# Kernel tuning notes

Hardware: AMD Instinct MI355X
Metric: run time of the kernel (lower is better)

The kernel has to match this reference:

```python
import jax, jax.numpy as jnp
import numpy as np

N = 50000      # nodes
E = 1600000    # edges (avg degree 32)
IN = 128       # input feature dim
H = 4          # heads
C = 16         # out channels per head
NEG_SLOPE = 0.2


def setup_inputs() -> dict:
    key = jax.random.key(0)
    k = jax.random.split(key, 6)
    x = jax.random.normal(k[0], (N, IN), jnp.float32)
    edge_index = jax.random.randint(k[1], (2, E), 0, N, dtype=jnp.int32).astype(jnp.int64)
    W = jax.random.normal(k[2], (H * C, IN), jnp.float32) * (1.0 / np.sqrt(IN))
    att_src = jax.random.normal(k[3], (H, C), jnp.float32) * 0.1
    att_dst = jax.random.normal(k[4], (H, C), jnp.float32) * 0.1
    bias = jax.random.normal(k[5], (H * C,), jnp.float32) * 0.01
    return {"x": x, "edge_index": edge_index, "W": W,
            "att_src": att_src, "att_dst": att_dst, "bias": bias}


def reference(x, edge_index, W, att_src, att_dst, bias):
    # shared linear projection (PyG GATConv lin, no bias): [N, H, C]
    xp = (x @ W.T).reshape(-1, H, C)
    # per-node attention logits: [N, H]
    a_src = jnp.einsum('nhc,hc->nh', xp, att_src)
    a_dst = jnp.einsum('nhc,hc->nh', xp, att_dst)
    src, dst = edge_index[0], edge_index[1]  # messages flow src(j) -> dst(i)
    # per-edge scores: [E, H]
    e = jax.nn.leaky_relu(a_src[src] + a_dst[dst], negative_slope=NEG_SLOPE)
    # segment softmax over destination neighborhoods
    m = jax.ops.segment_max(e, dst, num_segments=N)           # [N, H]
    m = jnp.where(jnp.isfinite(m), m, 0.0)                     # empty segments
    ex = jnp.exp(e - m[dst])
    s = jax.ops.segment_sum(ex, dst, num_segments=N)           # [N, H]
    alpha = ex / (s[dst] + 1e-16)                              # [E, H]
    # weighted messages, scatter-add to destinations
    msg = (alpha[:, :, None] * xp[src]).reshape(E, H * C)      # [E, H*C]
    out = jax.ops.segment_sum(msg, dst, num_segments=N)        # [N, H*C]
    return out + bias
```

## Files before the change

### kernel.cpp

```cpp
#include <hip/hip_runtime.h>
#include <hip/hip_bf16.h>
#include <math.h>

#define N_NODES 50000
#define N_EDGES 1600000
#define IN_DIM  128
#define HC      64
#define NH      4
#define SLOTS   72
#define BSHIFT  6
#define BNODES  64
#define NB      782
#define BCAP    2432
#define BIN_BLOCKS 64
#define BIN_G   6250
#define BIN_IT  13
#define GEMM_BLOCKS 391
#define GEMM_LDS 33792

__global__ __launch_bounds__(512) void bin_kernel(
    const int* __restrict__ ei, int* __restrict__ gcursor,
    unsigned int* __restrict__ barr) {
    __shared__ int lcount[NB], lbase[NB], lcnt2[NB];
    int tid = (int)threadIdx.x;
    int bx  = (int)blockIdx.x;
    for (int j = tid; j < NB; j += 512) { lcount[j] = 0; lcnt2[j] = 0; }
    __syncthreads();
    const int4* sp = (const int4*)ei;
    const int4* dp = (const int4*)(ei + N_EDGES);
    int g0 = bx * BIN_G;

    for (int it = 0; it < BIN_IT; ++it) {
        int gi = it * 512 + tid;
        if (gi < BIN_G) {
            int4 dv = dp[g0 + gi];
            atomicAdd(&lcount[dv.x >> BSHIFT], 1);
            atomicAdd(&lcount[dv.y >> BSHIFT], 1);
            atomicAdd(&lcount[dv.z >> BSHIFT], 1);
            atomicAdd(&lcount[dv.w >> BSHIFT], 1);
        }
    }
    __syncthreads();
    for (int j = tid; j < NB; j += 512) {
        int c = lcount[j];
        lbase[j] = (c > 0) ? atomicAdd(&gcursor[j], c) : 0;
    }
    __syncthreads();
    for (int it = 0; it < BIN_IT; ++it) {
        int gi = it * 512 + tid;
        if (gi < BIN_G) {
            int4 sv = sp[g0 + gi];
            int4 dv = dp[g0 + gi];
            int s[4] = {sv.x, sv.y, sv.z, sv.w};
            int d[4] = {dv.x, dv.y, dv.z, dv.w};
#pragma unroll
            for (int u = 0; u < 4; ++u) {
                int bk = d[u] >> BSHIFT;
                int lp = atomicAdd(&lcnt2[bk], 1);
                int pos = lbase[bk] + lp;
                if (pos < BCAP)
                    barr[(size_t)bk * BCAP + pos] =
                        (unsigned)s[u] | ((unsigned)(d[u] & (BNODES - 1)) << 20);
            }
        }
    }
}

__global__ __launch_bounds__(512) void gemm_kernel(
    const float* __restrict__ x, const float* __restrict__ W,
    const float* __restrict__ att_src, const float* __restrict__ att_dst,
    __hip_bfloat16* __restrict__ xp, float* __restrict__ a_src,
    float* __restrict__ a_dst) {
    extern __shared__ char smraw[];
    int tid = (int)threadIdx.x;
    int gb  = (int)blockIdx.x;
    float* Wl = (float*)smraw;
    const float4* W4 = (const float4*)W;
#pragma unroll
    for (int j = 0; j < 4; ++j) {
        int f = j * 512 + tid;
        int c = f >> 5, k4 = f & 31;
        *(float4*)&Wl[c * 132 + k4 * 4] = W4[f];
    }
    __syncthreads();

    int l = tid & 63, w = tid >> 6, q = l >> 4, i = l & 15;
    int n0 = gb * 128 + w * 16 + q * 4;
    int nj[4];
#pragma unroll
    for (int j = 0; j < 4; ++j) {
        int n = n0 + j;
        nj[j] = (n < N_NODES) ? n : N_NODES - 1;
    }
    const float* wlp = Wl + i * 132;
    float4 acc[4] = {{0,0,0,0},{0,0,0,0},{0,0,0,0},{0,0,0,0}};
    float4 xr[4], xn[4];
#pragma unroll
    for (int j = 0; j < 4; ++j) xr[j] = *(const float4*)(x + (size_t)nj[j] * IN_DIM);
#pragma unroll 2
    for (int k0 = 0; k0 < IN_DIM; k0 += 4) {
        if (k0 + 4 < IN_DIM) {
#pragma unroll
            for (int j = 0; j < 4; ++j)
                xn[j] = *(const float4*)(x + (size_t)nj[j] * IN_DIM + k0 + 4);
        }
        float4 wl0 = *(const float4*)(wlp + 0 * 16 * 132 + k0);
        float4 wl1 = *(const float4*)(wlp + 1 * 16 * 132 + k0);
        float4 wl2 = *(const float4*)(wlp + 2 * 16 * 132 + k0);
        float4 wl3 = *(const float4*)(wlp + 3 * 16 * 132 + k0);
#pragma unroll
        for (int j = 0; j < 4; ++j) {
            float4 xv = xr[j];
            acc[j].x = fmaf(xv.x, wl0.x, fmaf(xv.y, wl0.y, fmaf(xv.z, wl0.z, fmaf(xv.w, wl0.w, acc[j].x))));
            acc[j].y = fmaf(xv.x, wl1.x, fmaf(xv.y, wl1.y, fmaf(xv.z, wl1.z, fmaf(xv.w, wl1.w, acc[j].y))));
            acc[j].z = fmaf(xv.x, wl2.x, fmaf(xv.y, wl2.y, fmaf(xv.z, wl2.z, fmaf(xv.w, wl2.w, acc[j].z))));
            acc[j].w = fmaf(xv.x, wl3.x, fmaf(xv.y, wl3.y, fmaf(xv.z, wl3.z, fmaf(xv.w, wl3.w, acc[j].w))));
        }
#pragma unroll
        for (int j = 0; j < 4; ++j) xr[j] = xn[j];
    }

    float a_s0 = att_src[i], a_s1 = att_src[16 + i], a_s2 = att_src[32 + i], a_s3 = att_src[48 + i];
    float a_d0 = att_dst[i], a_d1 = att_dst[16 + i], a_d2 = att_dst[32 + i], a_d3 = att_dst[48 + i];
#pragma unroll
    for (int j = 0; j < 4; ++j) {
        int n = n0 + j;
        if (n < N_NODES) {
            __hip_bfloat16* xw = xp + (size_t)n * HC;
            xw[i]      = __float2bfloat16(acc[j].x);
            xw[16 + i] = __float2bfloat16(acc[j].y);
            xw[32 + i] = __float2bfloat16(acc[j].z);
            xw[48 + i] = __float2bfloat16(acc[j].w);
            float4 ps, pd;
            ps.x = acc[j].x * a_s0; ps.y = acc[j].y * a_s1;
            ps.z = acc[j].z * a_s2; ps.w = acc[j].w * a_s3;
            pd.x = acc[j].x * a_d0; pd.y = acc[j].y * a_d1;
            pd.z = acc[j].z * a_d2; pd.w = acc[j].w * a_d3;
#pragma unroll
            for (int off = 1; off < 16; off <<= 1) {
                ps.x += __shfl_xor(ps.x, off, 64); ps.y += __shfl_xor(ps.y, off, 64);
                ps.z += __shfl_xor(ps.z, off, 64); ps.w += __shfl_xor(ps.w, off, 64);
                pd.x += __shfl_xor(pd.x, off, 64); pd.y += __shfl_xor(pd.y, off, 64);
                pd.z += __shfl_xor(pd.z, off, 64); pd.w += __shfl_xor(pd.w, off, 64);
            }
            if (i == 0) {
                *(float4*)(a_src + n * NH) = ps;
                *(float4*)(a_dst + n * NH) = pd;
            }
        }
    }
}

__global__ __launch_bounds__(512) void fused_gather_kernel(
    const unsigned int* __restrict__ barr, const int* __restrict__ gcursor,
    const float* __restrict__ a_src, const float* __restrict__ a_dst,
    const __hip_bfloat16* __restrict__ xp, const float* __restrict__ bias,
    float* __restrict__ out) {
    __shared__ int lcsr[BNODES * SLOTS];
    __shared__ int deg[BNODES];
    int b = blockIdx.x, tid = (int)threadIdx.x;
    if (tid < BNODES) deg[tid] = 0;
    __syncthreads();
    int n = gcursor[b];
    n = (n < BCAP) ? n : BCAP;
    const unsigned int* src = barr + (size_t)b * BCAP;

    for (int i0 = 0; i0 < n; i0 += 2048) {
        int ibase = i0 + tid * 4;
        unsigned v[4]; bool val[4]; int dp[4], pos[4];
        if (ibase < n) {
            uint4 r = *(const uint4*)(src + ibase);
            v[0] = r.x; v[1] = r.y; v[2] = r.z; v[3] = r.w;
        } else { v[0] = v[1] = v[2] = v[3] = 0u; }
#pragma unroll
        for (int u = 0; u < 4; ++u) {
            val[u] = (ibase + u) < n;
            dp[u] = (int)(v[u] >> 20);
            if (val[u]) pos[u] = atomicAdd(&deg[dp[u]], 1);
        }
#pragma unroll
        for (int u = 0; u < 4; ++u)
            if (val[u] && pos[u] < SLOTS)
                lcsr[dp[u] * SLOTS + pos[u]] = (int)(v[u] & 0xFFFFF);
    }
    __syncthreads();

    int l = tid & 63;
    int w = tid >> 6;
    int g = l >> 3;
    int i = l & 7;
    int h = i >> 1;
    int dl = w * 8 + g;
    int dst = (b << BSHIFT) + dl;
    int dg = deg[dl];
    dg = (dg < SLOTS) ? dg : SLOTS;
    int dstc = (dst < N_NODES) ? dst : 0;
    float adh = a_dst[dstc * NH + h];

    int sreg[9];
#pragma unroll
    for (int k = 0; k < 9; ++k) sreg[k] = lcsr[dl * SLOTS + k * 8 + i];

    const unsigned short* xpi = (const unsigned short*)xp + 8 * i;
    const float* asrch = a_src + h;
    int gsel = l & 56;
    float a0=0,a1=0,a2=0,a3=0,a4=0,a5=0,a6=0,a7=0;
    float dsum = 0.f;

#pragma unroll
    for (int k = 0; k < 9; ++k) {
        if (dg > k * 8) {
            int cnt = dg - k * 8;
            int reg = sreg[k];
            int s8[8]; float g8[8]; uint4 t8[8];
#pragma unroll
            for (int u = 0; u < 8; ++u) {
                int raw = __shfl(reg, gsel | u, 64);
                s8[u] = (u < cnt) ? raw : 0;
            }
#pragma unroll
            for (int u = 0; u < 8; ++u) g8[u] = asrch[s8[u] * NH];
#pragma unroll
            for (int u = 0; u < 8; ++u)
                t8[u] = *(const uint4*)(xpi + (size_t)s8[u] * HC);
#pragma unroll
            for (int u = 0; u < 8; ++u) {
                float e = g8[u] + adh;
                e = fmaxf(e, 0.2f * e);
                float wv = (u < cnt) ? __expf(e) : 0.f;
                dsum += wv;
                uint4 t = t8[u];
                a0 = fmaf(wv, __uint_as_float(t.x << 16),          a0);
                a1 = fmaf(wv, __uint_as_float(t.x & 0xffff0000u),  a1);
                a2 = fmaf(wv, __uint_as_float(t.y << 16),          a2);
                a3 = fmaf(wv, __uint_as_float(t.y & 0xffff0000u),  a3);
                a4 = fmaf(wv, __uint_as_float(t.z << 16),          a4);
                a5 = fmaf(wv, __uint_as_float(t.z & 0xffff0000u),  a5);
                a6 = fmaf(wv, __uint_as_float(t.w << 16),          a6);
                a7 = fmaf(wv, __uint_as_float(t.w & 0xffff0000u),  a7);
            }
        }
    }
    if (dst < N_NODES) {
        float inv = 1.f / (dsum + 1e-16f);
        float4 b0 = *(const float4*)(bias + 8 * i);
        float4 b1 = *(const float4*)(bias + 8 * i + 4);
        float4 o0, o1;
        o0.x = a0 * inv + b0.x; o0.y = a1 * inv + b0.y;
        o0.z = a2 * inv + b0.z; o0.w = a3 * inv + b0.w;
        o1.x = a4 * inv + b1.x; o1.y = a5 * inv + b1.y;
        o1.z = a6 * inv + b1.z; o1.w = a7 * inv + b1.w;
        float* op = out + (size_t)dst * HC + 8 * i;
        *(float4*)op = o0;
        *(float4*)(op + 4) = o1;
    }
}

extern "C" void kernel_launch(void* const* d_in, const int* in_sizes, int n_in,
                              void* d_out, int out_size, void* d_ws, size_t ws_size,
                              hipStream_t stream) {
    const float* x       = (const float*)d_in[0];
    const int*   ei      = (const int*)d_in[1];
    const float* W       = (const float*)d_in[2];
    const float* att_src = (const float*)d_in[3];
    const float* att_dst = (const float*)d_in[4];
    const float* bias    = (const float*)d_in[5];
    float* out = (float*)d_out;

    char* ws = (char*)d_ws;
    __hip_bfloat16* xp      = (__hip_bfloat16*)(ws);
    float*          a_srcv  = (float*)(ws + 6400000);
    float*          a_dstv  = (float*)(ws + 7200000);
    int*            gcursor = (int*)  (ws + 8000000);
    unsigned int*   barr    = (unsigned int*)(ws + 8016384);

    hipMemsetAsync(gcursor, 0, NB * sizeof(int), stream);
    bin_kernel<<<BIN_BLOCKS, 512, 0, stream>>>(ei, gcursor, barr);
    gemm_kernel<<<GEMM_BLOCKS, 512, GEMM_LDS, stream>>>(
        x, W, att_src, att_dst, xp, a_srcv, a_dstv);
    fused_gather_kernel<<<NB, 512, 0, stream>>>(barr, gcursor,
                                                a_srcv, a_dstv, xp, bias, out);
}
```

Before: 167.8 us.

## Split edge binning into count, scan and append kernels with more blocks

Replaces the single binning kernel, which used 64 blocks and global atomic cursors, with three kernels. A per-block count pass, a per-bucket exclusive scan across blocks, and an append pass that writes at precomputed offsets. Block count rises from 64 to 250 to fill more of the GPU, and the memset and global atomics go away. The cost is two extra kernel launches, a second read of the destination indices, and a counts/base matrix in workspace. Bucket order within a bin also becomes deterministic.

```diff
diff --git a/kernel.cpp b/kernel.cpp
--- a/kernel.cpp
+++ b/kernel.cpp
@@ -12,25 +12,22 @@
 #define BNODES  64
 #define NB      782
 #define BCAP    2432
-#define BIN_BLOCKS 64
-#define BIN_G   6250
-#define BIN_IT  13
+#define BIN_BLOCKS 250
+#define BIN_G   1600
 #define GEMM_BLOCKS 391
 #define GEMM_LDS 33792
 
-__global__ __launch_bounds__(512) void bin_kernel(
-    const int* __restrict__ ei, int* __restrict__ gcursor,
-    unsigned int* __restrict__ barr) {
-    __shared__ int lcount[NB], lbase[NB], lcnt2[NB];
+__global__ __launch_bounds__(512) void bin_count_kernel(
+    const int* __restrict__ ei, int* __restrict__ counts) {
+    __shared__ int lcount[NB];
     int tid = (int)threadIdx.x;
     int bx  = (int)blockIdx.x;
-    for (int j = tid; j < NB; j += 512) { lcount[j] = 0; lcnt2[j] = 0; }
-    __syncthreads();
-    const int4* sp = (const int4*)ei;
+    for (int j = tid; j < NB; j += 512) lcount[j] = 0;
+    __syncthreads();
     const int4* dp = (const int4*)(ei + N_EDGES);
     int g0 = bx * BIN_G;
-
-    for (int it = 0; it < BIN_IT; ++it) {
+#pragma unroll
+    for (int it = 0; it < 4; ++it) {
         int gi = it * 512 + tid;
         if (gi < BIN_G) {
             int4 dv = dp[g0 + gi];
@@ -41,12 +38,45 @@
         }
     }
     __syncthreads();
+    for (int j = tid; j < NB; j += 512)
+        counts[bx * NB + j] = lcount[j];
+}
+
+__global__ __launch_bounds__(256) void bin_scan_kernel(
+    const int* __restrict__ counts, int* __restrict__ base,
+    int* __restrict__ btot) {
+    __shared__ int sc[256];
+    int j = (int)blockIdx.x, t = (int)threadIdx.x;
+    int v = (t < BIN_BLOCKS) ? counts[t * NB + j] : 0;
+    sc[t] = v;
+    __syncthreads();
+#pragma unroll
+    for (int off = 1; off < 256; off <<= 1) {
+        int u = (t >= off) ? sc[t - off] : 0;
+        __syncthreads();
+        sc[t] += u;
+        __syncthreads();
+    }
+    if (t < BIN_BLOCKS) base[t * NB + j] = sc[t] - v;
+    if (t == BIN_BLOCKS - 1) btot[j] = sc[t];
+}
+
+__global__ __launch_bounds__(512) void bin_append_kernel(
+    const int* __restrict__ ei, const int* __restrict__ base,
+    unsigned int* __restrict__ barr) {
+    __shared__ int lbase[NB], lcnt[NB];
+    int tid = (int)threadIdx.x;
+    int bx  = (int)blockIdx.x;
     for (int j = tid; j < NB; j += 512) {
-        int c = lcount[j];
-        lbase[j] = (c > 0) ? atomicAdd(&gcursor[j], c) : 0;
-    }
-    __syncthreads();
-    for (int it = 0; it < BIN_IT; ++it) {
+        lbase[j] = base[bx * NB + j];
+        lcnt[j]  = 0;
+    }
+    __syncthreads();
+    const int4* sp = (const int4*)ei;
+    const int4* dp = (const int4*)(ei + N_EDGES);
+    int g0 = bx * BIN_G;
+#pragma unroll
+    for (int it = 0; it < 4; ++it) {
         int gi = it * 512 + tid;
         if (gi < BIN_G) {
             int4 sv = sp[g0 + gi];
@@ -56,7 +86,7 @@
 #pragma unroll
             for (int u = 0; u < 4; ++u) {
                 int bk = d[u] >> BSHIFT;
-                int lp = atomicAdd(&lcnt2[bk], 1);
+                int lp = atomicAdd(&lcnt[bk], 1);
                 int pos = lbase[bk] + lp;
                 if (pos < BCAP)
                     barr[(size_t)bk * BCAP + pos] =
@@ -152,7 +182,7 @@
 }
 
 __global__ __launch_bounds__(512) void fused_gather_kernel(
-    const unsigned int* __restrict__ barr, const int* __restrict__ gcursor,
+    const unsigned int* __restrict__ barr, const int* __restrict__ btot,
     const float* __restrict__ a_src, const float* __restrict__ a_dst,
     const __hip_bfloat16* __restrict__ xp, const float* __restrict__ bias,
     float* __restrict__ out) {
@@ -161,7 +191,7 @@
     int b = blockIdx.x, tid = (int)threadIdx.x;
     if (tid < BNODES) deg[tid] = 0;
     __syncthreads();
-    int n = gcursor[b];
+    int n = btot[b];
     n = (n < BCAP) ? n : BCAP;
     const unsigned int* src = barr + (size_t)b * BCAP;
 
@@ -271,13 +301,16 @@
     __hip_bfloat16* xp      = (__hip_bfloat16*)(ws);
     float*          a_srcv  = (float*)(ws + 6400000);
     float*          a_dstv  = (float*)(ws + 7200000);
-    int*            gcursor = (int*)  (ws + 8000000);
+    int*            btot    = (int*)  (ws + 8000000);
     unsigned int*   barr    = (unsigned int*)(ws + 8016384);
-
-    hipMemsetAsync(gcursor, 0, NB * sizeof(int), stream);
-    bin_kernel<<<BIN_BLOCKS, 512, 0, stream>>>(ei, gcursor, barr);
+    int*            counts  = (int*)  (ws + 15624192);
+    int*            basem   = (int*)  (ws + 16406272);
+
+    bin_count_kernel<<<BIN_BLOCKS, 512, 0, stream>>>(ei, counts);
+    bin_scan_kernel<<<NB, 256, 0, stream>>>(counts, basem, btot);
+    bin_append_kernel<<<BIN_BLOCKS, 512, 0, stream>>>(ei, basem, barr);
     gemm_kernel<<<GEMM_BLOCKS, 512, GEMM_LDS, stream>>>(
         x, W, att_src, att_dst, xp, a_srcv, a_dstv);
-    fused_gather_kernel<<<NB, 512, 0, stream>>>(barr, gcursor,
+    fused_gather_kernel<<<NB, 512, 0, stream>>>(barr, btot,
                                                 a_srcv, a_dstv, xp, bias, out);
 }
```

New measurement: 153.2 us. 1.1x faster.
